# Performance work log

Measured on AMD Instinct MI355X. Metric: run time of the kernel, lower is better.

## Reference

```python
import jax, jax.numpy as jnp
import numpy as np

CAUSAL = True

def setup_inputs() -> dict:
    key = jax.random.key(0)
    kq, kk, kv = jax.random.split(key, 3)
    B, S, H, D = 2, 2048, 16, 64
    q = jax.random.normal(kq, (B, S, H, D), dtype=jnp.float32)
    k = jax.random.normal(kk, (B, S, H, D), dtype=jnp.float32)
    v = jax.random.normal(kv, (B, S, H, D), dtype=jnp.float32)
    return {"q": q, "k": k, "v": v}

def reference(q, k, v):
    # q,k,v: [B, S, H, D]
    B, Sq, H, D = q.shape
    Sk = k.shape[1]
    scale = 1.0 / jnp.sqrt(jnp.asarray(D, dtype=q.dtype))
    # scores: [B, H, Sq, Sk]
    scores = jnp.einsum('bqhd,bkhd->bhqk', q * scale, k)
    if CAUSAL:
        causal_mask = jnp.triu(jnp.ones((Sq, Sk), dtype=bool), k=1)
        scores = jnp.where(causal_mask, -jnp.inf, scores)
    attn = jax.nn.softmax(scores, axis=-1)
    # output: [B, Sq, H, D]
    out = jnp.einsum('bhqk,bkhd->bqhd', attn, v)
    return out
```

## Files before the change

### kernel.cpp

```cpp
#include <hip/hip_runtime.h>


typedef __bf16  bf16x8_t  __attribute__((ext_vector_type(8)));
typedef short   short4_t  __attribute__((ext_vector_type(4)));
typedef float   f32x4     __attribute__((ext_vector_type(4)));

#define MFMA_K32(a, b, c) __builtin_amdgcn_mfma_f32_16x16x32_bf16((a), (b), (c), 0, 0, 0)

__device__ __forceinline__ f32x4 mfma_k16(short4_t a, short4_t b, f32x4 c) {
#if defined(__HIP_DEVICE_COMPILE__)
    return __builtin_amdgcn_mfma_f32_16x16x16bf16_1k(a, b, c, 0, 0, 0);
#else
    return c;
#endif
}

constexpr int   SEQ = 2048, NH = 16;
constexpr int   SROW = NH * 64;
constexpr float QS   = 0.125f * 1.44269504088896f;

__device__ __forceinline__ unsigned f2bfu(float f) {
    unsigned u = __builtin_bit_cast(unsigned, f);
    return (u + 0x7fffu + ((u >> 16) & 1u)) >> 16;
}
__device__ __forceinline__ unsigned pk2(float x, float y) {
#if defined(__HIP_DEVICE_COMPILE__) && __has_builtin(__builtin_amdgcn_cvt_pk_bf16_f32)
    typedef __bf16 bfv2 __attribute__((ext_vector_type(2)));
    bfv2 v = __builtin_amdgcn_cvt_pk_bf16_f32(x, y);
    return __builtin_bit_cast(unsigned, v);
#else
    return (f2bfu(x) & 0xffffu) | (f2bfu(y) << 16);
#endif
}

__global__ __launch_bounds__(256) void prepack(const float* __restrict__ K,
                                               const float* __restrict__ V,
                                               unsigned short* __restrict__ Kp,
                                               unsigned short* __restrict__ Vp) {
    const int blk = blockIdx.x;
    const int tid = threadIdx.x;
    if (blk < 1024) {
        const int bh = blk >> 5, c = blk & 31;
        const int b  = bh >> 4,  h = bh & 15;
        const int nt = tid >> 6, lane = tid & 63;
        const int llo = lane & 15, lhi = lane >> 4;
        const float* src = K + (size_t)(b * SEQ + c * 64 + nt * 16 + llo) * SROW + h * 64;
#pragma unroll
        for (int ks = 0; ks < 2; ++ks) {
            const float4* p = (const float4*)(src + ks * 32 + lhi * 8);
            float4 a = p[0], d4 = p[1];
            uint4 u;
            u.x = pk2(a.x, a.y);   u.y = pk2(a.z, a.w);
            u.z = pk2(d4.x, d4.y); u.w = pk2(d4.z, d4.w);
            *(uint4*)(Kp + (size_t)(bh * 32 + c) * 4096 + (nt * 2 + ks) * 512 + lane * 8) = u;
        }
    } else {
        const int q  = blk - 1024;
        const int bh = q >> 5, c = q & 31;
        const int b  = bh >> 4, h = bh & 15;
        const int dt = tid >> 6, lane = tid & 63;
        const int llo = lane & 15, lhi = lane >> 4;
        const float* src = V + (size_t)(b * SEQ + c * 64 + lhi * 4) * SROW + h * 64 + dt * 16 + llo;
#pragma unroll
        for (int kq = 0; kq < 4; ++kq) {
            const float* s2 = src + (size_t)(kq * 16) * SROW;
            float f0 = s2[0], f1 = s2[SROW], f2 = s2[2 * SROW], f3 = s2[3 * SROW];
            uint2 u;
            u.x = pk2(f0, f1); u.y = pk2(f2, f3);
            *(uint2*)(Vp + (size_t)(bh * 32 + c) * 4096 + (kq * 4 + dt) * 256 + lane * 4) = u;
        }
    }
}

__global__ __launch_bounds__(256, 5) void fa_fwd(const float* __restrict__ Q,
                                                 const unsigned short* __restrict__ Kp,
                                                 const unsigned short* __restrict__ Vp,
                                                 float* __restrict__ O) {
    const int id = blockIdx.x;
    const int bh = id & 31;
    const int T  = 63 - (id >> 5);
    const int b  = bh >> 4, h = bh & 15;
    const int iters = (T >> 1) + 1;
    const int q0    = T * 32;

    const int tid  = threadIdx.x;
    const int w    = tid >> 6;
    const int lane = tid & 63;
    const int lhi  = lane >> 4;
    const int llo  = lane & 15;

    __shared__ __align__(16) float Red[4][5][64][4];

    const char* Ku = (const char*)Kp + ((size_t)bh << 18);
    const char* Vu = (const char*)Vp + ((size_t)bh << 18);
    int kov = (w << 11) + lane * 16;
    int vov = (w << 11) + lane * 8;

    bf16x8_t qf[2][2];
#pragma unroll
    for (int mt = 0; mt < 2; ++mt)
#pragma unroll
        for (int ks = 0; ks < 2; ++ks) {
            const float* qp = Q + (size_t)(b * SEQ + q0 + mt * 16 + llo) * SROW + h * 64 + ks * 32 + lhi * 8;
            float4 a = ((const float4*)qp)[0], c4 = ((const float4*)qp)[1];
            uint4 u;
            u.x = pk2(a.x * QS, a.y * QS); u.y = pk2(a.z * QS, a.w * QS);
            u.z = pk2(c4.x * QS, c4.y * QS); u.w = pk2(c4.z * QS, c4.w * QS);
            qf[mt][ks] = __builtin_bit_cast(bf16x8_t, u);
        }

    f32x4 acc[2][4], accL[2];
#pragma unroll
    for (int mt = 0; mt < 2; ++mt) {
        accL[mt] = (f32x4){0.f, 0.f, 0.f, 0.f};
#pragma unroll
        for (int dt = 0; dt < 4; ++dt) acc[mt][dt] = (f32x4){0.f, 0.f, 0.f, 0.f};
    }

    short4_t ones;
#pragma unroll
    for (int j = 0; j < 4; ++j) ones[j] = (short)0x3F80;

    uint4 kc0 = *(const uint4*)(Ku + kov);
    uint4 kc1 = *(const uint4*)(Ku + kov + 1024);

    for (int kt = 0; kt < iters; ++kt) {
        uint4 kn0 = *(const uint4*)(Ku + kov + 8192);
        uint4 kn1 = *(const uint4*)(Ku + kov + 9216);

        uint2 vc[4];
#pragma unroll
        for (int dt = 0; dt < 4; ++dt)
            vc[dt] = *(const uint2*)(Vu + vov + dt * 512);

        f32x4 s[2];
#pragma unroll
        for (int mt = 0; mt < 2; ++mt) {
            f32x4 z = (f32x4){0.f, 0.f, 0.f, 0.f};
            z = MFMA_K32(__builtin_bit_cast(bf16x8_t, kc0), qf[mt][0], z);
            z = MFMA_K32(__builtin_bit_cast(bf16x8_t, kc1), qf[mt][1], z);
            s[mt] = z;
        }

        const int kv0 = kt << 6;
#pragma unroll
        for (int mt = 0; mt < 2; ++mt) {
            if (kv0 + w * 16 + 15 > q0 + mt * 16) {
                const int m_g = q0 + mt * 16 + llo;
#pragma unroll
                for (int r = 0; r < 4; ++r)
                    if (kv0 + w * 16 + lhi * 4 + r > m_g) s[mt][r] = -INFINITY;
            }
        }

        short4_t pf[2];
#pragma unroll
        for (int mt = 0; mt < 2; ++mt) {
            uint2 u = make_uint2(
                pk2(__builtin_amdgcn_exp2f(s[mt][0]), __builtin_amdgcn_exp2f(s[mt][1])),
                pk2(__builtin_amdgcn_exp2f(s[mt][2]), __builtin_amdgcn_exp2f(s[mt][3])));
            pf[mt] = __builtin_bit_cast(short4_t, u);
        }

#pragma unroll
        for (int dt = 0; dt < 4; ++dt) {
            short4_t vf = __builtin_bit_cast(short4_t, vc[dt]);
            acc[0][dt] = mfma_k16(pf[0], vf, acc[0][dt]);
            acc[1][dt] = mfma_k16(pf[1], vf, acc[1][dt]);
        }
        accL[0] = mfma_k16(pf[0], ones, accL[0]);
        accL[1] = mfma_k16(pf[1], ones, accL[1]);

        kov += 8192;
        vov += 8192;
        kc0 = kn0; kc1 = kn1;
    }

#pragma unroll
    for (int mt = 0; mt < 2; ++mt) {
#pragma unroll
        for (int dt = 0; dt < 4; ++dt) *(f32x4*)&Red[w][dt][lane][0] = acc[mt][dt];
        *(f32x4*)&Red[w][4][lane][0] = accL[mt];
        __syncthreads();
        f32x4 oc = (f32x4){0.f, 0.f, 0.f, 0.f};
        f32x4 ls = (f32x4){0.f, 0.f, 0.f, 0.f};
#pragma unroll
        for (int u = 0; u < 4; ++u) {
            oc += *(const f32x4*)&Red[u][w][lane][0];
            ls += *(const f32x4*)&Red[u][4][lane][0];
        }
#pragma unroll
        for (int r = 0; r < 4; ++r)
            O[(size_t)(b * SEQ + q0 + mt * 16 + lhi * 4 + r) * SROW + h * 64 + w * 16 + llo] = oc[r] / ls[r];
        __syncthreads();
    }
}

extern "C" void kernel_launch(void* const* d_in, const int* in_sizes, int n_in,
                              void* d_out, int out_size, void* d_ws, size_t ws_size,
                              hipStream_t stream) {
    const float* q = (const float*)d_in[0];
    const float* k = (const float*)d_in[1];
    const float* v = (const float*)d_in[2];
    float* o = (float*)d_out;
    unsigned short* Kp = (unsigned short*)d_ws;
    unsigned short* Vp = Kp + (size_t)32 * 32 * 4096;
    prepack<<<dim3(2048), dim3(256), 0, stream>>>(k, v, Kp, Vp);
    fa_fwd<<<dim3(2048), dim3(256), 0, stream>>>(q, Kp, Vp, o);
}
```

Before: 145.7 us.

## Double-buffer K/V tiles with unroll-by-two and repack V for wide loads

The main loop is unrolled by two so the next K and V tiles are prefetched into registers while the current tile is computed. The V prepack layout is changed so each lane fetches its four d-tile fragments with two 16-byte loads instead of four 8-byte loads. On odd iteration counts the loop runs one extra tile; causal masking zeroes its contribution, and V offsets are clamped to stay in range. Launch bounds drop from 5 to 4 blocks per CU to make room for the extra registers, which may cost latency hiding.

```diff
diff --git a/kernel.cpp b/kernel.cpp
--- a/kernel.cpp
+++ b/kernel.cpp
@@ -3,6 +3,7 @@
 
 typedef __bf16  bf16x8_t  __attribute__((ext_vector_type(8)));
 typedef short   short4_t  __attribute__((ext_vector_type(4)));
+typedef short   short8_t  __attribute__((ext_vector_type(8)));
 typedef float   f32x4     __attribute__((ext_vector_type(4)));
 
 #define MFMA_K32(a, b, c) __builtin_amdgcn_mfma_f32_16x16x32_bf16((a), (b), (c), 0, 0, 0)
@@ -67,12 +68,12 @@
             float f0 = s2[0], f1 = s2[SROW], f2 = s2[2 * SROW], f3 = s2[3 * SROW];
             uint2 u;
             u.x = pk2(f0, f1); u.y = pk2(f2, f3);
-            *(uint2*)(Vp + (size_t)(bh * 32 + c) * 4096 + (kq * 4 + dt) * 256 + lane * 4) = u;
-        }
-    }
-}
-
-__global__ __launch_bounds__(256, 5) void fa_fwd(const float* __restrict__ Q,
+            *(uint2*)(Vp + (size_t)(bh * 128 + c * 4 + kq) * 1024 + lane * 16 + dt * 4) = u;
+        }
+    }
+}
+
+__global__ __launch_bounds__(256, 4) void fa_fwd(const float* __restrict__ Q,
                                                  const unsigned short* __restrict__ Kp,
                                                  const unsigned short* __restrict__ Vp,
                                                  float* __restrict__ O) {
@@ -94,7 +95,8 @@
     const char* Ku = (const char*)Kp + ((size_t)bh << 18);
     const char* Vu = (const char*)Vp + ((size_t)bh << 18);
     int kov = (w << 11) + lane * 16;
-    int vov = (w << 11) + lane * 8;
+    int vov = (w << 11) + lane * 32;
+    const int vmax = (iters - 1) * 8192 + (w << 11) + lane * 32;
 
     bf16x8_t qf[2][2];
 #pragma unroll
@@ -121,27 +123,15 @@
 #pragma unroll
     for (int j = 0; j < 4; ++j) ones[j] = (short)0x3F80;
 
-    uint4 kc0 = *(const uint4*)(Ku + kov);
-    uint4 kc1 = *(const uint4*)(Ku + kov + 1024);
-
-    for (int kt = 0; kt < iters; ++kt) {
-        uint4 kn0 = *(const uint4*)(Ku + kov + 8192);
-        uint4 kn1 = *(const uint4*)(Ku + kov + 9216);
-
-        uint2 vc[4];
-#pragma unroll
-        for (int dt = 0; dt < 4; ++dt)
-            vc[dt] = *(const uint2*)(Vu + vov + dt * 512);
-
+    auto compute = [&](int kt, uint4 k0, uint4 k1, uint4 v0, uint4 v1) {
         f32x4 s[2];
 #pragma unroll
         for (int mt = 0; mt < 2; ++mt) {
             f32x4 z = (f32x4){0.f, 0.f, 0.f, 0.f};
-            z = MFMA_K32(__builtin_bit_cast(bf16x8_t, kc0), qf[mt][0], z);
-            z = MFMA_K32(__builtin_bit_cast(bf16x8_t, kc1), qf[mt][1], z);
+            z = MFMA_K32(__builtin_bit_cast(bf16x8_t, k0), qf[mt][0], z);
+            z = MFMA_K32(__builtin_bit_cast(bf16x8_t, k1), qf[mt][1], z);
             s[mt] = z;
         }
-
         const int kv0 = kt << 6;
 #pragma unroll
         for (int mt = 0; mt < 2; ++mt) {
@@ -152,7 +142,6 @@
                     if (kv0 + w * 16 + lhi * 4 + r > m_g) s[mt][r] = -INFINITY;
             }
         }
-
         short4_t pf[2];
 #pragma unroll
         for (int mt = 0; mt < 2; ++mt) {
@@ -161,19 +150,49 @@
                 pk2(__builtin_amdgcn_exp2f(s[mt][2]), __builtin_amdgcn_exp2f(s[mt][3])));
             pf[mt] = __builtin_bit_cast(short4_t, u);
         }
-
+        short8_t va = __builtin_bit_cast(short8_t, v0);
+        short8_t vb = __builtin_bit_cast(short8_t, v1);
+        short4_t vf[4];
+        vf[0] = __builtin_shufflevector(va, va, 0, 1, 2, 3);
+        vf[1] = __builtin_shufflevector(va, va, 4, 5, 6, 7);
+        vf[2] = __builtin_shufflevector(vb, vb, 0, 1, 2, 3);
+        vf[3] = __builtin_shufflevector(vb, vb, 4, 5, 6, 7);
 #pragma unroll
         for (int dt = 0; dt < 4; ++dt) {
-            short4_t vf = __builtin_bit_cast(short4_t, vc[dt]);
-            acc[0][dt] = mfma_k16(pf[0], vf, acc[0][dt]);
-            acc[1][dt] = mfma_k16(pf[1], vf, acc[1][dt]);
+            acc[0][dt] = mfma_k16(pf[0], vf[dt], acc[0][dt]);
+            acc[1][dt] = mfma_k16(pf[1], vf[dt], acc[1][dt]);
         }
         accL[0] = mfma_k16(pf[0], ones, accL[0]);
         accL[1] = mfma_k16(pf[1], ones, accL[1]);
-
-        kov += 8192;
-        vov += 8192;
-        kc0 = kn0; kc1 = kn1;
+    };
+
+    uint4 kA0 = *(const uint4*)(Ku + kov);
+    uint4 kA1 = *(const uint4*)(Ku + kov + 1024);
+    uint4 vA0 = *(const uint4*)(Vu + vov);
+    uint4 vA1 = *(const uint4*)(Vu + vov + 16);
+    int kovn = kov + 8192;
+    int vovn = min(vov + 8192, vmax);
+
+    const int P = (iters + 1) >> 1;
+    for (int p = 0; p < P; ++p) {
+        const int kt0 = p * 2;
+        uint4 kB0 = *(const uint4*)(Ku + kovn);
+        uint4 kB1 = *(const uint4*)(Ku + kovn + 1024);
+        uint4 vB0 = *(const uint4*)(Vu + vovn);
+        uint4 vB1 = *(const uint4*)(Vu + vovn + 16);
+
+        compute(kt0, kA0, kA1, vA0, vA1);
+
+        kov += 16384;
+        vov = min(vov + 16384, vmax);
+        kA0 = *(const uint4*)(Ku + kov);
+        kA1 = *(const uint4*)(Ku + kov + 1024);
+        vA0 = *(const uint4*)(Vu + vov);
+        vA1 = *(const uint4*)(Vu + vov + 16);
+        kovn += 16384;
+        vovn = min(vov + 8192, vmax);
+
+        compute(kt0 + 1, kB0, kB1, vB0, vB1);
     }
 
 #pragma unroll
```

Measured after the change: 124.9 us. -14.3%, faster.

## Process 128-key superchunks per iteration using K32 MFMAs for PV

Applied to the files above, without the earlier changes.

Each warp now handles 32 keys per iteration instead of 16, so a 128-key superchunk is covered per loop step, and the PV and rowsum products use the 16x16x32 bf16 MFMA instead of the 16x16x16 variant. V is prepacked in a new 32-key-group layout that matches the wider B fragment, loaded as uint4 per lane. The change halves loop trip count and MFMA issue count for PV, and in exchange raises register pressure, so the occupancy hint drops from 5 to 4. Causal masking work per step may grow slightly because the trip count is rounded up to the superchunk.

```diff
diff --git a/kernel.cpp b/kernel.cpp
--- a/kernel.cpp
+++ b/kernel.cpp
@@ -2,18 +2,11 @@
 
 
 typedef __bf16  bf16x8_t  __attribute__((ext_vector_type(8)));
-typedef short   short4_t  __attribute__((ext_vector_type(4)));
+typedef short   short8_t  __attribute__((ext_vector_type(8)));
 typedef float   f32x4     __attribute__((ext_vector_type(4)));
 
 #define MFMA_K32(a, b, c) __builtin_amdgcn_mfma_f32_16x16x32_bf16((a), (b), (c), 0, 0, 0)
-
-__device__ __forceinline__ f32x4 mfma_k16(short4_t a, short4_t b, f32x4 c) {
-#if defined(__HIP_DEVICE_COMPILE__)
-    return __builtin_amdgcn_mfma_f32_16x16x16bf16_1k(a, b, c, 0, 0, 0);
-#else
-    return c;
-#endif
-}
+#define BC8(x) __builtin_bit_cast(bf16x8_t, (x))
 
 constexpr int   SEQ = 2048, NH = 16;
 constexpr int   SROW = NH * 64;
@@ -60,19 +53,24 @@
         const int b  = bh >> 4, h = bh & 15;
         const int dt = tid >> 6, lane = tid & 63;
         const int llo = lane & 15, lhi = lane >> 4;
-        const float* src = V + (size_t)(b * SEQ + c * 64 + lhi * 4) * SROW + h * 64 + dt * 16 + llo;
-#pragma unroll
-        for (int kq = 0; kq < 4; ++kq) {
-            const float* s2 = src + (size_t)(kq * 16) * SROW;
-            float f0 = s2[0], f1 = s2[SROW], f2 = s2[2 * SROW], f3 = s2[3 * SROW];
-            uint2 u;
+#pragma unroll
+        for (int g2 = 0; g2 < 2; ++g2) {
+            const int g = c * 2 + g2;
+            const float* base = V + (size_t)(b * SEQ + g * 32 + 4 * lhi) * SROW + h * 64 + dt * 16 + llo;
+            float f0 = base[0],            f1 = base[SROW],
+                  f2 = base[2 * SROW],     f3 = base[3 * SROW];
+            const float* b2 = base + 16 * SROW;
+            float f4 = b2[0],              f5 = b2[SROW],
+                  f6 = b2[2 * SROW],       f7 = b2[3 * SROW];
+            uint4 u;
             u.x = pk2(f0, f1); u.y = pk2(f2, f3);
-            *(uint2*)(Vp + (size_t)(bh * 32 + c) * 4096 + (kq * 4 + dt) * 256 + lane * 4) = u;
-        }
-    }
-}
-
-__global__ __launch_bounds__(256, 5) void fa_fwd(const float* __restrict__ Q,
+            u.z = pk2(f4, f5); u.w = pk2(f6, f7);
+            *(uint4*)(Vp + (size_t)(bh * 64 + g) * 2048 + dt * 512 + lane * 8) = u;
+        }
+    }
+}
+
+__global__ __launch_bounds__(256, 4) void fa_fwd(const float* __restrict__ Q,
                                                  const unsigned short* __restrict__ Kp,
                                                  const unsigned short* __restrict__ Vp,
                                                  float* __restrict__ O) {
@@ -80,8 +78,8 @@
     const int bh = id & 31;
     const int T  = 63 - (id >> 5);
     const int b  = bh >> 4, h = bh & 15;
-    const int iters = (T >> 1) + 1;
-    const int q0    = T * 32;
+    const int NSC = (T + 4) >> 2;
+    const int q0  = T * 32;
 
     const int tid  = threadIdx.x;
     const int w    = tid >> 6;
@@ -93,8 +91,8 @@
 
     const char* Ku = (const char*)Kp + ((size_t)bh << 18);
     const char* Vu = (const char*)Vp + ((size_t)bh << 18);
-    int kov = (w << 11) + lane * 16;
-    int vov = (w << 11) + lane * 8;
+    int kov = (w << 12) + lane * 16;
+    int vov = (w << 12) + lane * 16;
 
     bf16x8_t qf[2][2];
 #pragma unroll
@@ -117,63 +115,64 @@
         for (int dt = 0; dt < 4; ++dt) acc[mt][dt] = (f32x4){0.f, 0.f, 0.f, 0.f};
     }
 
-    short4_t ones;
-#pragma unroll
-    for (int j = 0; j < 4; ++j) ones[j] = (short)0x3F80;
-
-    uint4 kc0 = *(const uint4*)(Ku + kov);
-    uint4 kc1 = *(const uint4*)(Ku + kov + 1024);
-
-    for (int kt = 0; kt < iters; ++kt) {
-        uint4 kn0 = *(const uint4*)(Ku + kov + 8192);
-        uint4 kn1 = *(const uint4*)(Ku + kov + 9216);
-
-        uint2 vc[4];
-#pragma unroll
-        for (int dt = 0; dt < 4; ++dt)
-            vc[dt] = *(const uint2*)(Vu + vov + dt * 512);
-
-        f32x4 s[2];
+    short8_t o8;
+#pragma unroll
+    for (int j = 0; j < 8; ++j) o8[j] = (short)0x3F80;
+    const bf16x8_t ones8 = __builtin_bit_cast(bf16x8_t, o8);
+
+    uint4 kc[4];
+#pragma unroll
+    for (int i = 0; i < 4; ++i) kc[i] = *(const uint4*)(Ku + kov + i * 1024);
+
+    for (int sc = 0; sc < NSC; ++sc) {
+        uint4 kn[4];
+#pragma unroll
+        for (int i = 0; i < 4; ++i) kn[i] = *(const uint4*)(Ku + kov + 16384 + i * 1024);
+        uint4 vc[4];
+#pragma unroll
+        for (int dt = 0; dt < 4; ++dt) vc[dt] = *(const uint4*)(Vu + vov + dt * 1024);
+
+        const int kb = (sc << 7) + (w << 5);
+
 #pragma unroll
         for (int mt = 0; mt < 2; ++mt) {
-            f32x4 z = (f32x4){0.f, 0.f, 0.f, 0.f};
-            z = MFMA_K32(__builtin_bit_cast(bf16x8_t, kc0), qf[mt][0], z);
-            z = MFMA_K32(__builtin_bit_cast(bf16x8_t, kc1), qf[mt][1], z);
-            s[mt] = z;
-        }
-
-        const int kv0 = kt << 6;
-#pragma unroll
-        for (int mt = 0; mt < 2; ++mt) {
-            if (kv0 + w * 16 + 15 > q0 + mt * 16) {
-                const int m_g = q0 + mt * 16 + llo;
+            f32x4 s0 = (f32x4){0.f, 0.f, 0.f, 0.f};
+            f32x4 s1 = (f32x4){0.f, 0.f, 0.f, 0.f};
+            s0 = MFMA_K32(BC8(kc[0]), qf[mt][0], s0);
+            s0 = MFMA_K32(BC8(kc[1]), qf[mt][1], s0);
+            s1 = MFMA_K32(BC8(kc[2]), qf[mt][0], s1);
+            s1 = MFMA_K32(BC8(kc[3]), qf[mt][1], s1);
+
+            const int m0 = q0 + mt * 16;
+            const int m_g = m0 + llo;
+            if (kb + 15 > m0) {
 #pragma unroll
                 for (int r = 0; r < 4; ++r)
-                    if (kv0 + w * 16 + lhi * 4 + r > m_g) s[mt][r] = -INFINITY;
+                    if (kb + lhi * 4 + r > m_g) s0[r] = -INFINITY;
             }
-        }
-
-        short4_t pf[2];
-#pragma unroll
-        for (int mt = 0; mt < 2; ++mt) {
-            uint2 u = make_uint2(
-                pk2(__builtin_amdgcn_exp2f(s[mt][0]), __builtin_amdgcn_exp2f(s[mt][1])),
-                pk2(__builtin_amdgcn_exp2f(s[mt][2]), __builtin_amdgcn_exp2f(s[mt][3])));
-            pf[mt] = __builtin_bit_cast(short4_t, u);
-        }
-
-#pragma unroll
-        for (int dt = 0; dt < 4; ++dt) {
-            short4_t vf = __builtin_bit_cast(short4_t, vc[dt]);
-            acc[0][dt] = mfma_k16(pf[0], vf, acc[0][dt]);
-            acc[1][dt] = mfma_k16(pf[1], vf, acc[1][dt]);
-        }
-        accL[0] = mfma_k16(pf[0], ones, accL[0]);
-        accL[1] = mfma_k16(pf[1], ones, accL[1]);
-
-        kov += 8192;
-        vov += 8192;
-        kc0 = kn0; kc1 = kn1;
+            if (kb + 31 > m0) {
+#pragma unroll
+                for (int r = 0; r < 4; ++r)
+                    if (kb + 16 + lhi * 4 + r > m_g) s1[r] = -INFINITY;
+            }
+
+            uint4 up;
+            up.x = pk2(__builtin_amdgcn_exp2f(s0[0]), __builtin_amdgcn_exp2f(s0[1]));
+            up.y = pk2(__builtin_amdgcn_exp2f(s0[2]), __builtin_amdgcn_exp2f(s0[3]));
+            up.z = pk2(__builtin_amdgcn_exp2f(s1[0]), __builtin_amdgcn_exp2f(s1[1]));
+            up.w = pk2(__builtin_amdgcn_exp2f(s1[2]), __builtin_amdgcn_exp2f(s1[3]));
+            const bf16x8_t pf = BC8(up);
+
+#pragma unroll
+            for (int dt = 0; dt < 4; ++dt)
+                acc[mt][dt] = MFMA_K32(pf, BC8(vc[dt]), acc[mt][dt]);
+            accL[mt] = MFMA_K32(pf, ones8, accL[mt]);
+        }
+
+        kov += 16384;
+        vov += 16384;
+#pragma unroll
+        for (int i = 0; i < 4; ++i) kc[i] = kn[i];
     }
 
 #pragma unroll
```

Measured after the change: 134.4 us. -7.7%, faster.
